# Performance work log

Hardware: AMD Instinct MI355X
Metric: run time of the kernel (lower is better)

Reference implementation:

```python
import jax, jax.numpy as jnp
import numpy as np

B, T, H, V = 256, 256, 512, 32000
L = 3  # stacked LSTM layers


def setup_inputs() -> dict:
    key = jax.random.key(0)
    ks = jax.random.split(key, 12)
    s = 0.05
    n = lambda k, shp: (jax.random.normal(k, shp, jnp.float32) * s)
    return {
        "text_1": jax.random.randint(ks[0], (B, T), 0, V, dtype=jnp.int32),
        "text_2": jax.random.randint(ks[1], (B, T), 0, V, dtype=jnp.int32),
        "text_3": jax.random.randint(ks[2], (B, T), 0, V, dtype=jnp.int32),
        "emb": n(ks[3], (V, H)),
        "Wx": n(ks[4], (L, H, 4 * H)),
        "Wh": n(ks[5], (L, H, 4 * H)),
        "b": jnp.zeros((L, 4 * H), jnp.float32),
        "g1": jnp.ones((3 * H,), jnp.float32), "beta1": jnp.zeros((3 * H,), jnp.float32),
        "W1": n(ks[6], (3 * H, 2 * H)), "bd1": jnp.zeros((2 * H,), jnp.float32),
        "g2": jnp.ones((2 * H,), jnp.float32), "beta2": jnp.zeros((2 * H,), jnp.float32),
        "W2": n(ks[7], (2 * H, H // 5)), "bd2": jnp.zeros((H // 5,), jnp.float32),
        "g3": jnp.ones((H // 5,), jnp.float32), "beta3": jnp.zeros((H // 5,), jnp.float32),
        "W3": n(ks[8], (H // 5, 4)), "bd3": jnp.zeros((4,), jnp.float32),
    }


def _lstm_stack(tokens, emb, Wx, Wh, b):
    # tokens: [B, T] int -> last hidden of top layer [B, H]
    x = emb[tokens]                      # [B, T, H]
    x = jnp.transpose(x, (1, 0, 2))      # [T, B, H] (scan over time)
    bsz, h = x.shape[1], Wh.shape[1]
    for l in range(Wx.shape[0]):
        Wx_l, Wh_l, b_l = Wx[l], Wh[l], b[l]
        def step(carry, xt):
            hprev, cprev = carry
            gates = xt @ Wx_l + hprev @ Wh_l + b_l      # [B, 4H]
            i, f, g, o = jnp.split(gates, 4, axis=-1)
            c = jax.nn.sigmoid(f) * cprev + jax.nn.sigmoid(i) * jnp.tanh(g)
            hnew = jax.nn.sigmoid(o) * jnp.tanh(c)
            return (hnew, c), hnew
        init = (jnp.zeros((bsz, h), x.dtype), jnp.zeros((bsz, h), x.dtype))
        _, x = jax.lax.scan(step, init, x)
    return x[-1]                          # rnn_output[:, -1, :]


def _bn(x, gamma, beta, eps=1e-3):
    m = jnp.mean(x, axis=0)
    v = jnp.var(x, axis=0)
    return gamma * (x - m) * jax.lax.rsqrt(v + eps) + beta


def reference(text_1, text_2, text_3, emb, Wx, Wh, b,
              g1, beta1, W1, bd1, g2, beta2, W2, bd2, g3, beta3, W3, bd3):
    r1 = _lstm_stack(text_1, emb, Wx, Wh, b)
    r2 = _lstm_stack(text_2, emb, Wx, Wh, b)
    r3 = _lstm_stack(text_3, emb, Wx, Wh, b)
    r = jnp.concatenate([r1, r2, r3], axis=1)   # [B, 3H]
    r = _bn(r, g1, beta1)
    r = jax.nn.selu(r @ W1 + bd1)
    r = _bn(r, g2, beta2)
    r = jax.nn.selu(r @ W2 + bd2)
    r = _bn(r, g3, beta3)
    return r @ W3 + bd3                          # [B, 4] logits
```

## Files before the change

### kernel.cpp

```cpp
#include <hip/hip_runtime.h>
#include <hip/hip_bf16.h>

typedef __attribute__((ext_vector_type(8))) short short8;
typedef __attribute__((ext_vector_type(4))) float floatx4;

namespace {
constexpr int kB1 = 256;
constexpr int kT  = 256;
constexpr int kH  = 512;
constexpr int kL  = 3;
constexpr int kB3 = 768;
constexpr int kK  = 1024;
constexpr int kN  = 2048;
constexpr size_t kHB = (size_t)kB3 * kH;

constexpr size_t WREP_OFF   = 0;
constexpr size_t WREP_BYTES = (size_t)kL * kK * kN * 2;
constexpr size_t BREP_OFF   = WREP_OFF + WREP_BYTES;
constexpr size_t BREP_BYTES = (size_t)kL * kN * 4;
constexpr size_t HBUF_OFF   = BREP_OFF + BREP_BYTES;
constexpr size_t HBUF_BYTES = (size_t)kL * 2 * kHB * 2;
constexpr size_t CBUF_OFF   = HBUF_OFF + HBUF_BYTES;
constexpr size_t CBUF_BYTES = (size_t)kL * kHB * 4;
constexpr size_t BNA_OFF    = CBUF_OFF + CBUF_BYTES;
constexpr size_t BNC_OFF    = BNA_OFF + 1536 * 4;
constexpr size_t Z1_OFF     = BNC_OFF + 1536 * 4;
constexpr size_t Z2_OFF     = Z1_OFF + (size_t)256 * 1024 * 4;
constexpr size_t FLAG_OFF   = Z2_OFF + (size_t)256 * 102 * 4;
}

__device__ __forceinline__ float ldf(const void* p, size_t idx, int isf32) {
  if (isf32) return ((const float*)p)[idx];
  return __bfloat162float(((const __hip_bfloat16*)p)[idx]);
}

__device__ __forceinline__ short f2bs(float x) {
  union { __hip_bfloat16 h; short s; } u;
  u.h = __float2bfloat16(x);
  return u.s;
}

__global__ void detect_kernel(const unsigned* __restrict__ g1, int* __restrict__ flag) {
  if (threadIdx.x == 0 && blockIdx.x == 0)
    *flag = (g1[0] == 0x3F800000u) ? 1 : 0;
}

__global__ __launch_bounds__(256) void repack_kernel(
    const void* __restrict__ Wx, const void* __restrict__ Wh,
    const void* __restrict__ bias, const int* __restrict__ flagp,
    __hip_bfloat16* __restrict__ Wrep, float* __restrict__ brep) {
  int isf32 = *flagp;
  int idx = blockIdx.x * 256 + threadIdx.x;
  if (idx >= kL * kK * kN) return;
  int j  = idx & 7;
  int n2 = (idx >> 3) & (kN - 1);
  int kg = (idx >> 14) & 127;
  int l  = idx >> 21;
  int k  = kg * 8 + j;
  int ntile = n2 >> 7, c = n2 & 127, g = c >> 5, ul = c & 31;
  int u = ntile * 32 + ul;
  int col = g * 512 + u;
  float v;
  if (k < kH) v = ldf(Wx, ((size_t)l * kH + k) * kN + col, isf32);
  else        v = ldf(Wh, ((size_t)l * kH + (k - kH)) * kN + col, isf32);
  Wrep[idx] = __float2bfloat16(v);
  if (kg == 0 && j == 0) brep[l * kN + n2] = ldf(bias, (size_t)l * kN + col, isf32);
}

__global__ __launch_bounds__(256) void step_kernel(
    int s,
    const __hip_bfloat16* __restrict__ Wrep, const float* __restrict__ brep,
    __hip_bfloat16* __restrict__ hbuf, float* __restrict__ cbuf,
    const void* __restrict__ emb, const int* __restrict__ flagp,
    const int* __restrict__ t1, const int* __restrict__ t2, const int* __restrict__ t3) {
  __shared__ __align__(16) char smem[34816];

  int bid = blockIdx.x;
  int l  = bid / 192;
  int rr = bid % 192;
  int nt = rr & 15;
  int mt = rr >> 4;
  int t = s - l;
  if (t < 0 || t >= kT) return;

  int isf32 = *flagp;
  int tid = threadIdx.x;
  int wv = tid >> 6, lane = tid & 63;
  int lm = lane & 15, lq = lane >> 4;

  int arow = tid >> 2;
  int kc   = tid & 3;
  int row_g = mt * 64 + arow;

  const void* xsrc;
  bool xf32 = false;
  if (l == 0) {
    int i = row_g >> 8, bb = row_g & 255;
    const int* txt = (i == 0) ? t1 : (i == 1) ? t2 : t3;
    int tok = txt[bb * kT + t];
    if (isf32) { xsrc = (const void*)((const float*)emb + (size_t)tok * kH); xf32 = true; }
    else         xsrc = (const void*)((const __hip_bfloat16*)emb + (size_t)tok * kH);
  } else {
    const __hip_bfloat16* hIn = hbuf + ((size_t)(l - 1) * 2 + (t & 1)) * kHB;
    xsrc = (const void*)(hIn + (size_t)row_g * kH);
  }
  const __hip_bfloat16* hrow = nullptr;
  if (t > 0) {
    const __hip_bfloat16* hPrev = hbuf + ((size_t)l * 2 + ((t & 1) ^ 1)) * kHB;
    hrow = hPrev + (size_t)row_g * kH;
  }

  floatx4 zf = {0.f, 0.f, 0.f, 0.f};
  floatx4 acc[4][2];
#pragma unroll
  for (int a = 0; a < 4; a++)
#pragma unroll
    for (int b = 0; b < 2; b++) acc[a][b] = zf;

  const __hip_bfloat16* WB = Wrep + (size_t)l * kK * kN;
  int n0w = nt * 128 + wv * 32;

#pragma unroll 1
  for (int sl = 0; sl < 8; sl++) {
    short8 bfrag[4][2];
#pragma unroll
    for (int kk = 0; kk < 4; kk++)
#pragma unroll
      for (int nf = 0; nf < 2; nf++) {
        size_t kg = (size_t)(sl * 16 + kk * 4 + lq);
        const __hip_bfloat16* p = WB + (kg * kN + (n0w + nf * 16 + lm)) * 8;
        bfrag[kk][nf] = *(const short8*)p;
      }
    short8 av[4];
    bool zero = (sl >= 4) && (t == 0);
    if (!zero) {
      if (sl < 4 && xf32) {
        const float* sf = (const float*)xsrc + sl * 128;
#pragma unroll
        for (int jj = 0; jj < 4; jj++) {
          const float* q = sf + kc * 8 + jj * 32;
          float4 lo = *(const float4*)q;
          float4 hi = *(const float4*)(q + 4);
          short8 v;
          v[0] = f2bs(lo.x); v[1] = f2bs(lo.y); v[2] = f2bs(lo.z); v[3] = f2bs(lo.w);
          v[4] = f2bs(hi.x); v[5] = f2bs(hi.y); v[6] = f2bs(hi.z); v[7] = f2bs(hi.w);
          av[jj] = v;
        }
      } else {
        const __hip_bfloat16* src = (sl < 4)
            ? ((const __hip_bfloat16*)xsrc + sl * 128)
            : (hrow + (sl - 4) * 128);
#pragma unroll
        for (int jj = 0; jj < 4; jj++)
          av[jj] = *(const short8*)(src + kc * 8 + jj * 32);
      }
    } else {
      short8 vz = {0, 0, 0, 0, 0, 0, 0, 0};
#pragma unroll
      for (int jj = 0; jj < 4; jj++) av[jj] = vz;
    }
    __syncthreads();
#pragma unroll
    for (int jj = 0; jj < 4; jj++) {
      int klocal = kc * 8 + jj * 32;
      *(short8*)(smem + arow * 272 + klocal * 2) = av[jj];
    }
    __syncthreads();
#pragma unroll
    for (int kk = 0; kk < 4; kk++) {
      short8 afrag[4];
#pragma unroll
      for (int mf = 0; mf < 4; mf++) {
        int rowf = mf * 16 + lm;
        afrag[mf] = *(const short8*)(smem + rowf * 272 + kk * 64 + lq * 16);
      }
#pragma unroll
      for (int mf = 0; mf < 4; mf++)
#pragma unroll
        for (int nf = 0; nf < 2; nf++)
          acc[mf][nf] = __builtin_amdgcn_mfma_f32_16x16x32_bf16(
              afrag[mf], bfrag[kk][nf], acc[mf][nf], 0, 0, 0);
    }
  }

  const float* bl = brep + l * kN;
#pragma unroll
  for (int nf = 0; nf < 2; nf++) {
    float bv = bl[n0w + nf * 16 + lm];
#pragma unroll
    for (int mf = 0; mf < 4; mf++)
#pragma unroll
      for (int r = 0; r < 4; r++) acc[mf][nf][r] += bv;
  }

  __syncthreads();
  float* gl = (float*)smem;
#pragma unroll
  for (int mf = 0; mf < 4; mf++)
#pragma unroll
    for (int nf = 0; nf < 2; nf++)
#pragma unroll
      for (int r = 0; r < 4; r++) {
        int rowf = mf * 16 + lq * 4 + r;
        int uu   = nf * 16 + lm;
        gl[((size_t)wv * 64 + rowf) * 34 + uu] = acc[mf][nf][r];
      }
  __syncthreads();

  float* cl = cbuf + (size_t)l * kHB;
  __hip_bfloat16* hout = hbuf + ((size_t)l * 2 + (t & 1)) * kHB;
#pragma unroll
  for (int ii = 0; ii < 8; ii++) {
    int idx = tid + 256 * ii;
    int uu = idx & 31, rowf = idx >> 5;
    float gi = fminf(fmaxf(gl[(0 * 64 + rowf) * 34 + uu], -40.f), 40.f);
    float gf = fminf(fmaxf(gl[(1 * 64 + rowf) * 34 + uu], -40.f), 40.f);
    float gg = fminf(fmaxf(gl[(2 * 64 + rowf) * 34 + uu], -40.f), 40.f);
    float go = fminf(fmaxf(gl[(3 * 64 + rowf) * 34 + uu], -40.f), 40.f);
    int bg = mt * 64 + rowf;
    int ug = nt * 32 + uu;
    size_t off = (size_t)bg * kH + ug;
    float c_old = (t > 0) ? cl[off] : 0.f;
    float si = 1.f / (1.f + __expf(-gi));
    float sf = 1.f / (1.f + __expf(-gf));
    float so = 1.f / (1.f + __expf(-go));
    float cn = sf * c_old + si * tanhf(gg);
    float hn = so * tanhf(cn);
    cl[off] = cn;
    hout[off] = __float2bfloat16(hn);
  }
}

__global__ __launch_bounds__(256) void stats_kernel(
    int ncols, int mode, const void* __restrict__ src,
    const void* __restrict__ gamma, const void* __restrict__ beta,
    const int* __restrict__ flagp, float* __restrict__ bn_a, float* __restrict__ bn_c) {
  int isf32 = *flagp;
  int col = blockIdx.x * 256 + threadIdx.x;
  if (col >= ncols) return;
  float sum = 0.f, ss = 0.f;
  for (int b = 0; b < kB1; b++) {
    float v;
    if (mode == 0) {
      const __hip_bfloat16* h = (const __hip_bfloat16*)src;
      v = __bfloat162float(h[((size_t)((col >> 9) * kB1 + b)) * kH + (col & 511)]);
    } else {
      v = ((const float*)src)[(size_t)b * ncols + col];
    }
    v = fmaxf(-1e15f, fminf(v, 1e15f));
    sum += v; ss += v * v;
  }
  float mean = sum * (1.f / kB1);
  float var  = ss * (1.f / kB1) - mean * mean;
  float a = ldf(gamma, col, isf32) * rsqrtf(var + 1e-3f);
  bn_a[col] = a;
  bn_c[col] = ldf(beta, col, isf32) - mean * a;
}

__global__ __launch_bounds__(256) void headgemm_kernel(
    int Kd, int Nd, int mode, const void* __restrict__ Asrc,
    const float* __restrict__ bn_a, const float* __restrict__ bn_c,
    const void* __restrict__ W, const void* __restrict__ bias,
    const int* __restrict__ flagp, float* __restrict__ out, int do_selu) {
  __shared__ float As[32][65];
  __shared__ float Bs[32][65];
  int isf32 = *flagp;
  int tid = threadIdx.x;
  int bx = blockIdx.x, by = blockIdx.y;
  int tx = tid & 15, ty = tid >> 4;
  float acc[4][4] = {};
  int am = tid & 63, ak = tid >> 6;
  int bk = tid >> 3, bn8 = (tid & 7) * 8;
  for (int ks = 0; ks < Kd; ks += 32) {
    __syncthreads();
    for (int jj = 0; jj < 8; jj++) {
      int kl = ak * 8 + jj;
      int kg = ks + kl;
      int mg = by * 64 + am;
      float v;
      if (mode == 0) {
        const __hip_bfloat16* h = (const __hip_bfloat16*)Asrc;
        v = __bfloat162float(h[((size_t)((kg >> 9) * kB1 + mg)) * kH + (kg & 511)]);
      } else {
        v = ((const float*)Asrc)[(size_t)mg * Kd + kg];
      }
      As[kl][am] = v * bn_a[kg] + bn_c[kg];
    }
    for (int e = 0; e < 8; e++) {
      int col = bx * 64 + bn8 + e;
      Bs[bk][bn8 + e] = (col < Nd) ? ldf(W, (size_t)(ks + bk) * Nd + col, isf32) : 0.f;
    }
    __syncthreads();
    for (int k = 0; k < 32; k++) {
      float ar[4], br[4];
#pragma unroll
      for (int i = 0; i < 4; i++) ar[i] = As[k][ty * 4 + i];
#pragma unroll
      for (int j = 0; j < 4; j++) br[j] = Bs[k][tx * 4 + j];
#pragma unroll
      for (int i = 0; i < 4; i++)
#pragma unroll
        for (int j = 0; j < 4; j++) acc[i][j] += ar[i] * br[j];
    }
  }
  for (int i = 0; i < 4; i++) {
    int row = by * 64 + ty * 4 + i;
    for (int j = 0; j < 4; j++) {
      int col = bx * 64 + tx * 4 + j;
      if (col < Nd) {
        float y = acc[i][j] + ldf(bias, col, isf32);
        if (do_selu)
          y = (y > 0.f) ? 1.0507009873554805f * y
                        : 1.0507009873554805f * 1.6732632423543772f * (__expf(y) - 1.f);
        out[(size_t)row * Nd + col] = y;
      }
    }
  }
}

__global__ __launch_bounds__(256) void final_kernel(
    const float* __restrict__ z2, const float* __restrict__ bn_a, const float* __restrict__ bn_c,
    const void* __restrict__ W3, const void* __restrict__ bd3,
    const int* __restrict__ flagp, void* __restrict__ out) {
  int isf32 = *flagp;
  int b = threadIdx.x;
  float acc[4] = {0.f, 0.f, 0.f, 0.f};
  for (int j = 0; j < 102; j++) {
    float y = z2[b * 102 + j] * bn_a[j] + bn_c[j];
#pragma unroll
    for (int g = 0; g < 4; g++) acc[g] += y * ldf(W3, j * 4 + g, isf32);
  }
#pragma unroll
  for (int g = 0; g < 4; g++) {
    float y = acc[g] + ldf(bd3, g, isf32);
    if (isf32) ((float*)out)[b * 4 + g] = y;
    else ((__hip_bfloat16*)out)[b * 4 + g] = __float2bfloat16(y);
  }
}

extern "C" void kernel_launch(void* const* d_in, const int* in_sizes, int n_in,
                              void* d_out, int out_size, void* d_ws, size_t ws_size,
                              hipStream_t stream) {
  const int* t1 = (const int*)d_in[0];
  const int* t2 = (const int*)d_in[1];
  const int* t3 = (const int*)d_in[2];
  const void* emb = d_in[3];
  const void* Wx  = d_in[4];
  const void* Wh  = d_in[5];
  const void* bb  = d_in[6];
  const void* g1  = d_in[7];
  const void* be1 = d_in[8];
  const void* W1  = d_in[9];
  const void* bd1 = d_in[10];
  const void* g2  = d_in[11];
  const void* be2 = d_in[12];
  const void* W2  = d_in[13];
  const void* bd2 = d_in[14];
  const void* g3  = d_in[15];
  const void* be3 = d_in[16];
  const void* W3  = d_in[17];
  const void* bd3 = d_in[18];

  char* ws = (char*)d_ws;
  __hip_bfloat16* Wrep = (__hip_bfloat16*)(ws + WREP_OFF);
  float* brep = (float*)(ws + BREP_OFF);
  __hip_bfloat16* hbuf = (__hip_bfloat16*)(ws + HBUF_OFF);
  float* cbuf = (float*)(ws + CBUF_OFF);
  float* bn_a = (float*)(ws + BNA_OFF);
  float* bn_c = (float*)(ws + BNC_OFF);
  float* z1 = (float*)(ws + Z1_OFF);
  float* z2 = (float*)(ws + Z2_OFF);
  int* flag = (int*)(ws + FLAG_OFF);

  detect_kernel<<<1, 64, 0, stream>>>((const unsigned*)g1, flag);

  repack_kernel<<<(kL * kK * kN) / 256, 256, 0, stream>>>(Wx, Wh, bb, flag, Wrep, brep);

  for (int s = 0; s < kT + kL - 1; s++)
    step_kernel<<<3 * 192, 256, 0, stream>>>(s, Wrep, brep, hbuf, cbuf, emb, flag, t1, t2, t3);

  const __hip_bfloat16* hTop = hbuf + (2 * 2 + 1) * kHB;
  stats_kernel<<<6, 256, 0, stream>>>(1536, 0, hTop, g1, be1, flag, bn_a, bn_c);
  headgemm_kernel<<<dim3(16, 4), 256, 0, stream>>>(1536, 1024, 0, hTop, bn_a, bn_c, W1, bd1, flag, z1, 1);
  stats_kernel<<<4, 256, 0, stream>>>(1024, 1, z1, g2, be2, flag, bn_a, bn_c);
  headgemm_kernel<<<dim3(2, 4), 256, 0, stream>>>(1024, 102, 1, z1, bn_a, bn_c, W2, bd2, flag, z2, 1);
  stats_kernel<<<1, 256, 0, stream>>>(102, 1, z2, g3, be3, flag, bn_a, bn_c);
  final_kernel<<<1, 256, 0, stream>>>(z2, bn_a, bn_c, W3, bd3, flag, (void*)d_out);
}
```

Baseline: 6.066 ms.

## Fuse repack and all LSTM timesteps into one persistent cooperative kernel

Replaces the 258 per-timestep kernel launches and the separate weight repack launch with a single cooperative persistent kernel that repacks the weights and then loops over wavefront steps, using grid-wide syncs between steps. This is meant to remove per-launch overhead and kernel-boundary drain for each step. The change also hoists the bias loads and token-row pointer out of the step, and replaces tanhf and division with fast exp/fdividef approximations. The old multi-launch path is kept as a fallback if occupancy is too low for a cooperative launch. Grid syncs have their own cost, and the fast tanh may overflow to NaN for large inputs (exp(2x) reaching inf gives inf/inf).

```diff
diff --git a/kernel.cpp b/kernel.cpp
--- a/kernel.cpp
+++ b/kernel.cpp
@@ -1,5 +1,8 @@
 #include <hip/hip_runtime.h>
 #include <hip/hip_bf16.h>
+#include <hip/hip_cooperative_groups.h>
+
+namespace cg = cooperative_groups;
 
 typedef __attribute__((ext_vector_type(8))) short short8;
 typedef __attribute__((ext_vector_type(4))) float floatx4;
@@ -9,10 +12,10 @@
 constexpr int kT  = 256;
 constexpr int kH  = 512;
 constexpr int kL  = 3;
-constexpr int kB3 = 768;
 constexpr int kK  = 1024;
 constexpr int kN  = 2048;
-constexpr size_t kHB = (size_t)kB3 * kH;
+constexpr int kGrid = 576;
+constexpr size_t kHB = (size_t)768 * kH;
 
 constexpr size_t WREP_OFF   = 0;
 constexpr size_t WREP_BYTES = (size_t)kL * kK * kN * 2;
@@ -40,64 +43,66 @@
   return u.s;
 }
 
+__device__ __forceinline__ float fast_tanh(float x) {
+  float e = __expf(2.f * x);
+  return __fdividef(e - 1.f, e + 1.f);
+}
+__device__ __forceinline__ float fast_sigmoid(float x) {
+  return __fdividef(1.f, 1.f + __expf(-x));
+}
+
 __global__ void detect_kernel(const unsigned* __restrict__ g1, int* __restrict__ flag) {
   if (threadIdx.x == 0 && blockIdx.x == 0)
     *flag = (g1[0] == 0x3F800000u) ? 1 : 0;
+}
+
+__device__ __forceinline__ void repack_body(
+    int start, int stride,
+    const void* __restrict__ Wx, const void* __restrict__ Wh,
+    const void* __restrict__ bias, int isf32,
+    __hip_bfloat16* __restrict__ Wrep, float* __restrict__ brep) {
+  for (int idx = start; idx < kL * kK * kN; idx += stride) {
+    int j  = idx & 7;
+    int n2 = (idx >> 3) & (kN - 1);
+    int kg = (idx >> 14) & 127;
+    int l  = idx >> 21;
+    int k  = kg * 8 + j;
+    int ntile = n2 >> 7, c = n2 & 127, g = c >> 5, ul = c & 31;
+    int u = ntile * 32 + ul;
+    int col = g * 512 + u;
+    float v;
+    if (k < kH) v = ldf(Wx, ((size_t)l * kH + k) * kN + col, isf32);
+    else        v = ldf(Wh, ((size_t)l * kH + (k - kH)) * kN + col, isf32);
+    Wrep[idx] = __float2bfloat16(v);
+    if (kg == 0 && j == 0) brep[l * kN + n2] = ldf(bias, (size_t)l * kN + col, isf32);
+  }
 }
 
 __global__ __launch_bounds__(256) void repack_kernel(
     const void* __restrict__ Wx, const void* __restrict__ Wh,
     const void* __restrict__ bias, const int* __restrict__ flagp,
     __hip_bfloat16* __restrict__ Wrep, float* __restrict__ brep) {
-  int isf32 = *flagp;
-  int idx = blockIdx.x * 256 + threadIdx.x;
-  if (idx >= kL * kK * kN) return;
-  int j  = idx & 7;
-  int n2 = (idx >> 3) & (kN - 1);
-  int kg = (idx >> 14) & 127;
-  int l  = idx >> 21;
-  int k  = kg * 8 + j;
-  int ntile = n2 >> 7, c = n2 & 127, g = c >> 5, ul = c & 31;
-  int u = ntile * 32 + ul;
-  int col = g * 512 + u;
-  float v;
-  if (k < kH) v = ldf(Wx, ((size_t)l * kH + k) * kN + col, isf32);
-  else        v = ldf(Wh, ((size_t)l * kH + (k - kH)) * kN + col, isf32);
-  Wrep[idx] = __float2bfloat16(v);
-  if (kg == 0 && j == 0) brep[l * kN + n2] = ldf(bias, (size_t)l * kN + col, isf32);
-}
-
-__global__ __launch_bounds__(256) void step_kernel(
-    int s,
-    const __hip_bfloat16* __restrict__ Wrep, const float* __restrict__ brep,
-    __hip_bfloat16* __restrict__ hbuf, float* __restrict__ cbuf,
-    const void* __restrict__ emb, const int* __restrict__ flagp,
-    const int* __restrict__ t1, const int* __restrict__ t2, const int* __restrict__ t3) {
-  __shared__ __align__(16) char smem[34816];
-
-  int bid = blockIdx.x;
-  int l  = bid / 192;
-  int rr = bid % 192;
-  int nt = rr & 15;
-  int mt = rr >> 4;
-  int t = s - l;
-  if (t < 0 || t >= kT) return;
-
-  int isf32 = *flagp;
-  int tid = threadIdx.x;
-  int wv = tid >> 6, lane = tid & 63;
-  int lm = lane & 15, lq = lane >> 4;
-
-  int arow = tid >> 2;
-  int kc   = tid & 3;
-  int row_g = mt * 64 + arow;
-
-  const void* xsrc;
-  bool xf32 = false;
+  repack_body(blockIdx.x * 256 + threadIdx.x, gridDim.x * 256, Wx, Wh, bias, *flagp,
+              Wrep, brep);
+}
+
+__device__ __forceinline__ void lstm_step(
+    int l, int mt, int nt, int t, int isf32,
+    const __hip_bfloat16* __restrict__ WB, float bv0, float bv1,
+    __hip_bfloat16* __restrict__ hbuf, float* __restrict__ cl,
+    const void* __restrict__ emb, const int* __restrict__ txt,
+    char* smem) {
+  const int tid = threadIdx.x;
+  const int wv = tid >> 6, lane = tid & 63;
+  const int lm = lane & 15, lq = lane >> 4;
+  const int arow = tid >> 2;
+  const int kc   = tid & 3;
+  const int row_g = mt * 64 + arow;
+  const int n0w = nt * 128 + wv * 32;
+
+  const void* xsrc;  bool xf32 = false;
   if (l == 0) {
-    int i = row_g >> 8, bb = row_g & 255;
-    const int* txt = (i == 0) ? t1 : (i == 1) ? t2 : t3;
-    int tok = txt[bb * kT + t];
+    int tok = txt[t];
     if (isf32) { xsrc = (const void*)((const float*)emb + (size_t)tok * kH); xf32 = true; }
     else         xsrc = (const void*)((const __hip_bfloat16*)emb + (size_t)tok * kH);
   } else {
@@ -116,9 +121,6 @@
   for (int a = 0; a < 4; a++)
 #pragma unroll
     for (int b = 0; b < 2; b++) acc[a][b] = zf;
-
-  const __hip_bfloat16* WB = Wrep + (size_t)l * kK * kN;
-  int n0w = nt * 128 + wv * 32;
 
 #pragma unroll 1
   for (int sl = 0; sl < 8; sl++) {
@@ -183,15 +185,13 @@
     }
   }
 
-  const float* bl = brep + l * kN;
-#pragma unroll
-  for (int nf = 0; nf < 2; nf++) {
-    float bv = bl[n0w + nf * 16 + lm];
-#pragma unroll
-    for (int mf = 0; mf < 4; mf++)
-#pragma unroll
-      for (int r = 0; r < 4; r++) acc[mf][nf][r] += bv;
-  }
+#pragma unroll
+  for (int mf = 0; mf < 4; mf++)
+#pragma unroll
+    for (int r = 0; r < 4; r++) {
+      acc[mf][0][r] += bv0;
+      acc[mf][1][r] += bv1;
+    }
 
   __syncthreads();
   float* gl = (float*)smem;
@@ -207,7 +207,6 @@
       }
   __syncthreads();
 
-  float* cl = cbuf + (size_t)l * kHB;
   __hip_bfloat16* hout = hbuf + ((size_t)l * 2 + (t & 1)) * kHB;
 #pragma unroll
   for (int ii = 0; ii < 8; ii++) {
@@ -215,20 +214,94 @@
     int uu = idx & 31, rowf = idx >> 5;
     float gi = fminf(fmaxf(gl[(0 * 64 + rowf) * 34 + uu], -40.f), 40.f);
     float gf = fminf(fmaxf(gl[(1 * 64 + rowf) * 34 + uu], -40.f), 40.f);
-    float gg = fminf(fmaxf(gl[(2 * 64 + rowf) * 34 + uu], -40.f), 40.f);
+    float gG = fminf(fmaxf(gl[(2 * 64 + rowf) * 34 + uu], -40.f), 40.f);
     float go = fminf(fmaxf(gl[(3 * 64 + rowf) * 34 + uu], -40.f), 40.f);
     int bg = mt * 64 + rowf;
     int ug = nt * 32 + uu;
     size_t off = (size_t)bg * kH + ug;
     float c_old = (t > 0) ? cl[off] : 0.f;
-    float si = 1.f / (1.f + __expf(-gi));
-    float sf = 1.f / (1.f + __expf(-gf));
-    float so = 1.f / (1.f + __expf(-go));
-    float cn = sf * c_old + si * tanhf(gg);
-    float hn = so * tanhf(cn);
+    float cn = fast_sigmoid(gf) * c_old + fast_sigmoid(gi) * fast_tanh(gG);
+    float hn = fast_sigmoid(go) * fast_tanh(cn);
     cl[off] = cn;
     hout[off] = __float2bfloat16(hn);
   }
+  __syncthreads();
+}
+
+__global__ __launch_bounds__(256, 3) void persist_kernel(
+    const void* __restrict__ Wx, const void* __restrict__ Wh,
+    const void* __restrict__ bias, const int* __restrict__ flagp,
+    __hip_bfloat16* __restrict__ Wrep, float* __restrict__ brep,
+    __hip_bfloat16* __restrict__ hbuf, float* __restrict__ cbuf,
+    const void* __restrict__ emb,
+    const int* __restrict__ t1, const int* __restrict__ t2, const int* __restrict__ t3) {
+  cg::grid_group gg = cg::this_grid();
+  __shared__ __align__(16) char smem[34816];
+
+  const int bid = blockIdx.x;
+  const int tid = threadIdx.x;
+  const int isf32 = *flagp;
+
+  repack_body(bid * 256 + tid, kGrid * 256, Wx, Wh, bias, isf32, Wrep, brep);
+  gg.sync();
+
+  const int l  = bid / 192;
+  const int rr = bid % 192;
+  const int nt = rr & 15;
+  const int mt = rr >> 4;
+  const __hip_bfloat16* const WB = Wrep + (size_t)l * kK * kN;
+  float* const cl = cbuf + (size_t)l * kHB;
+  const int n0w = nt * 128 + (tid >> 6) * 32;
+  const int lm = tid & 15;
+  const float bv0 = brep[l * kN + n0w + lm];
+  const float bv1 = brep[l * kN + n0w + 16 + lm];
+
+  const int* txt = nullptr;
+  if (l == 0) {
+    int row_g = mt * 64 + (tid >> 2);
+    int i = row_g >> 8;
+    txt = (i == 0) ? t1 : (i == 1) ? t2 : t3;
+    txt += (row_g & 255) * kT;
+  }
+
+  for (int s = 0; s < kT + kL - 1; s++) {
+    const int t = s - l;
+    if (t >= 0 && t < kT)
+      lstm_step(l, mt, nt, t, isf32, WB, bv0, bv1, hbuf, cl, emb, txt, smem);
+    gg.sync();
+  }
+}
+
+__global__ __launch_bounds__(256, 3) void step_kernel(
+    int s,
+    const __hip_bfloat16* __restrict__ Wrep, const float* __restrict__ brep,
+    __hip_bfloat16* __restrict__ hbuf, float* __restrict__ cbuf,
+    const void* __restrict__ emb, const int* __restrict__ flagp,
+    const int* __restrict__ t1, const int* __restrict__ t2, const int* __restrict__ t3) {
+  __shared__ __align__(16) char smem[34816];
+  const int bid = blockIdx.x;
+  const int l  = bid / 192;
+  const int rr = bid % 192;
+  const int nt = rr & 15;
+  const int mt = rr >> 4;
+  const int t = s - l;
+  if (t < 0 || t >= kT) return;
+  const int isf32 = *flagp;
+  const int tid = threadIdx.x;
+  const __hip_bfloat16* WB = Wrep + (size_t)l * kK * kN;
+  float* cl = cbuf + (size_t)l * kHB;
+  const int n0w = nt * 128 + (tid >> 6) * 32;
+  const int lm = tid & 15;
+  const float bv0 = brep[l * kN + n0w + lm];
+  const float bv1 = brep[l * kN + n0w + 16 + lm];
+  const int* txt = nullptr;
+  if (l == 0) {
+    int row_g = mt * 64 + (tid >> 2);
+    int i = row_g >> 8;
+    txt = (i == 0) ? t1 : (i == 1) ? t2 : t3;
+    txt += (row_g & 255) * kT;
+  }
+  lstm_step(l, mt, nt, t, isf32, WB, bv0, bv1, hbuf, cl, emb, txt, smem);
 }
 
 __global__ __launch_bounds__(256) void stats_kernel(
@@ -374,10 +447,32 @@
 
   detect_kernel<<<1, 64, 0, stream>>>((const unsigned*)g1, flag);
 
-  repack_kernel<<<(kL * kK * kN) / 256, 256, 0, stream>>>(Wx, Wh, bb, flag, Wrep, brep);
-
-  for (int s = 0; s < kT + kL - 1; s++)
-    step_kernel<<<3 * 192, 256, 0, stream>>>(s, Wrep, brep, hbuf, cbuf, emb, flag, t1, t2, t3);
+  bool coop_ok = false;
+  {
+    int numCU = 0, maxBlk = 0;
+    int dev = 0;
+    if (hipGetDevice(&dev) == hipSuccess &&
+        hipDeviceGetAttribute(&numCU, hipDeviceAttributeMultiprocessorCount, dev) == hipSuccess &&
+        hipOccupancyMaxActiveBlocksPerMultiprocessor(&maxBlk, (const void*)persist_kernel,
+                                                     256, 0) == hipSuccess) {
+      if ((long)maxBlk * numCU >= kGrid) {
+        void* args[] = {(void*)&Wx, (void*)&Wh, (void*)&bb, (void*)&flag,
+                        (void*)&Wrep, (void*)&brep, (void*)&hbuf, (void*)&cbuf,
+                        (void*)&emb, (void*)&t1, (void*)&t2, (void*)&t3};
+        hipError_t err = hipLaunchCooperativeKernel((const void*)persist_kernel,
+                                                    dim3(kGrid), dim3(256), args, 0, stream);
+        if (err == hipSuccess) coop_ok = true;
+        else (void)hipGetLastError();
+      }
+    } else {
+      (void)hipGetLastError();
+    }
+  }
+  if (!coop_ok) {
+    repack_kernel<<<(kL * kK * kN) / 256, 256, 0, stream>>>(Wx, Wh, bb, flag, Wrep, brep);
+    for (int s = 0; s < kT + kL - 1; s++)
+      step_kernel<<<kGrid, 256, 0, stream>>>(s, Wrep, brep, hbuf, cbuf, emb, flag, t1, t2, t3);
+  }
 
   const __hip_bfloat16* hTop = hbuf + (2 * 2 + 1) * kHB;
   stats_kernel<<<6, 256, 0, stream>>>(1536, 0, hTop, g1, be1, flag, bn_a, bn_c);
```

New measurement: 6.296 ms. 3.8% more time.
